# Kernel optimization log

Measured on AMD Instinct MI355X. Metric: run time of the kernel, lower is better.

## Reference

```python
import jax, jax.numpy as jnp
import numpy as np


def setup_inputs() -> dict:
    key = jax.random.key(0)
    k0, k1, k2, k3, k4 = jax.random.split(key, 5)
    B, H, Lq, Lk, D = 2, 8, 512, 512, 32
    q = jax.random.normal(k0, (B, H, Lq, D), dtype=jnp.float32)
    k = jax.random.normal(k1, (B, H, Lk, D), dtype=jnp.float32)
    scale = jnp.ones((1,), dtype=jnp.float32)  # accepted but unused by the module
    # mask True = padded / excluded (torch masked_fill semantics)
    mask = jax.random.bernoulli(k2, 0.1, (B, Lq, Lk))
    attn_bias = jax.random.normal(k3, (B, H, Lq, Lk), dtype=jnp.float32) * 0.1
    # GATv2 attention vector, torch shape (1,H,1,1,D) -> stored as (H,D)
    limit = float(np.sqrt(6.0 / (1.0 + D)))  # xavier_uniform fan_in=1*1*D? torch uses full shape; scale is immaterial for correctness
    attention = jax.random.uniform(k4, (H, D), dtype=jnp.float32, minval=-limit, maxval=limit)
    return {"q": q, "k": k, "scale": scale, "mask": mask, "attn_bias": attn_bias, "attention": attention}


def reference(q, k, scale, mask, attn_bias, attention):
    # q: [B,H,Lq,D], k: [B,H,Lk,D], attention: [H,D]
    # broadcast additive combine -> [B,H,Lq,Lk,D]
    summed = q[:, :, :, None, :] + k[:, :, None, :, :]
    # SiLU activation, dot with per-head attention vector, reduce D -> [B,H,Lq,Lk]
    scores = jnp.einsum("bhqkd,hd->bhqk", jax.nn.silu(summed), attention)
    scores = scores + attn_bias
    # masked softmax over Lk; mask broadcasts over heads (unsqueeze at -3)
    scores = jnp.where(mask[:, None, :, :], -jnp.inf, scores)
    w = jax.nn.softmax(scores, axis=-1)
    # rows that are fully masked produce NaN -> replace with 0 (torch nan_to_num)
    return jnp.nan_to_num(w, nan=0.0)
```

## Files before the change

### kernel.cpp

```cpp
#include <hip/hip_runtime.h>
#include <hip/hip_bf16.h>
#include <math.h>

#define BB 2
#define HH 8
#define LQ 512
#define LK 512
#define DD 32
#define D2 (DD / 2)
#define C2 2
#define NC (D2 / C2)
#define WAVES 8
#define RPW 2
#define ROWSPB (WAVES * RPW)

#define LOG2E 1.44269504088896f

static __device__ __forceinline__ float fast_rcp(float x) {
#if __has_builtin(__builtin_amdgcn_rcpf)
  return __builtin_amdgcn_rcpf(x);
#else
  return 1.0f / x;
#endif
}

static __device__ __forceinline__ float fast_exp2(float x) {
#if __has_builtin(__builtin_amdgcn_exp2f)
  return __builtin_amdgcn_exp2f(x);
#else
  return __expf(x * 0.69314718056f);
#endif
}

__global__ __launch_bounds__(256) void gatv2_prek_p(
    const float* __restrict__ k, const float* __restrict__ att,
    float4* __restrict__ wst4) {
  const int bh = blockIdx.x >> 3;
  const int kt = blockIdx.x & 7;
  const int h = bh & (HH - 1);
  const int t = threadIdx.x;

  __shared__ float tile[64][33];

  const float4* src = (const float4*)(k + ((size_t)bh * LK + kt * 64) * DD);
#pragma unroll
  for (int i = 0; i < 2; ++i) {
    const int idx = t + i * 256;
    const float4 v = src[idx];
    const int kkl = idx >> 3;
    const int d4 = (idx & 7) * 4;
    tile[kkl][d4 + 0] = v.x; tile[kkl][d4 + 1] = v.y;
    tile[kkl][d4 + 2] = v.z; tile[kkl][d4 + 3] = v.w;
  }
  __syncthreads();

  const int d2 = t >> 4;
  const int kl0 = (t & 15) * 4;
  const float a0 = att[h * DD + 2 * d2 + 0];
  const float a1 = att[h * DD + 2 * d2 + 1];
  float4* dst = wst4 + ((size_t)bh * D2 + d2) * LK + kt * 64 + kl0;
#pragma unroll
  for (int j = 0; j < 4; ++j) {
    const float k0 = tile[kl0 + j][2 * d2 + 0];
    const float k1 = tile[kl0 + j][2 * d2 + 1];
    float4 o;
    o.x = fast_exp2(-k0 * LOG2E); o.y = k0 * a0;
    o.z = fast_exp2(-k1 * LOG2E); o.w = k1 * a1;
    dst[j] = o;
  }
}

__global__ __launch_bounds__(512) void gatv2_main_r2(
    const float* __restrict__ q, const int* __restrict__ mask,
    const float* __restrict__ bias, const float* __restrict__ att,
    const float4* __restrict__ wst4, float* __restrict__ out) {
  const int lane = threadIdx.x & 63;
  const int wid = threadIdx.x >> 6;
  const int tid = threadIdx.x;
  const int rowbase = blockIdx.x * ROWSPB;
  const int bh = rowbase >> 9;
  const int b = rowbase >> 12;
  const int h = bh & (HH - 1);

  __shared__ float4 lds4[2][C2 * LK];
  __shared__ float4 cst4[ROWSPB][D2];

  const float4* __restrict__ kb = wst4 + (size_t)bh * (D2 * LK);

  float4 s0 = kb[tid];
  float4 s1 = kb[tid + 512];

  {
    const int rw = wid * RPW + (lane >> 5);
    const int d = lane & 31;
    const float qd = q[(size_t)(rowbase + rw) * DD + d];
    const float ad = att[h * DD + d];
    float2 c;
    c.x = fast_exp2(-qd * LOG2E);
    c.y = qd * ad;
    ((float2*)cst4)[rw * DD + d] = c;
  }
  lds4[0][tid] = s0;
  lds4[0][tid + 512] = s1;

  float acc[RPW][8];
#pragma unroll
  for (int j = 0; j < RPW; ++j)
#pragma unroll
    for (int c = 0; c < 8; ++c) acc[j][c] = 0.0f;

  float bv[RPW][8];
  int mv[RPW][8];

#pragma unroll
  for (int cc = 0; cc < NC; ++cc) {
    __syncthreads();

    float4 s0n, s1n;
    if (cc + 1 < NC) {
      const float4* src = kb + (size_t)(cc + 1) * (C2 * LK);
      s0n = src[tid];
      s1n = src[tid + 512];
    } else {
      const float* __restrict__ brow = bias + (size_t)rowbase * LK;
      const int* __restrict__ mrow = mask + ((size_t)(b * LQ) + (rowbase & (LQ - 1))) * LK;
#pragma unroll
      for (int j = 0; j < RPW; ++j) {
        const int rw = wid * RPW + j;
#pragma unroll
        for (int c = 0; c < 8; ++c) {
          bv[j][c] = brow[(size_t)rw * LK + lane + 64 * c];
          mv[j][c] = mrow[(size_t)rw * LK + lane + 64 * c];
        }
      }
    }

    const float4 c0A = cst4[wid * RPW + 0][cc * 2 + 0];
    const float4 c0B = cst4[wid * RPW + 0][cc * 2 + 1];
    const float4 c1A = cst4[wid * RPW + 1][cc * 2 + 0];
    const float4 c1B = cst4[wid * RPW + 1][cc * 2 + 1];

    const float4* __restrict__ buf = lds4[cc & 1];
#pragma unroll
    for (int d2l = 0; d2l < C2; ++d2l) {
      const float4 k0 = d2l ? c0B : c0A;
      const float4 k1 = d2l ? c1B : c1A;
      const float4* __restrict__ pd = buf + d2l * LK + lane;
#pragma unroll
      for (int c = 0; c < 8; ++c) {
        const float4 p = pd[64 * c];
        float u = fmaf(k0.x, p.x, 1.0f);
        float t = k0.y + p.y;
        acc[0][c] = fmaf(t, fast_rcp(u), acc[0][c]);
        u = fmaf(k0.z, p.z, 1.0f);
        t = k0.w + p.w;
        acc[0][c] = fmaf(t, fast_rcp(u), acc[0][c]);
        u = fmaf(k1.x, p.x, 1.0f);
        t = k1.y + p.y;
        acc[1][c] = fmaf(t, fast_rcp(u), acc[1][c]);
        u = fmaf(k1.z, p.z, 1.0f);
        t = k1.w + p.w;
        acc[1][c] = fmaf(t, fast_rcp(u), acc[1][c]);
      }
    }

    if (cc + 1 < NC) {
      float4* dst = lds4[(cc + 1) & 1];
      dst[tid] = s0n;
      dst[tid + 512] = s1n;
    }
  }

#pragma unroll
  for (int j = 0; j < RPW; ++j) {
    const int r = rowbase + wid * RPW + j;

    float sc[8];
#pragma unroll
    for (int c = 0; c < 8; ++c)
      sc[c] = mv[j][c] ? -INFINITY : (acc[j][c] + bv[j][c]);

    float m = sc[0];
#pragma unroll
    for (int c = 1; c < 8; ++c) m = fmaxf(m, sc[c]);
#pragma unroll
    for (int off = 32; off > 0; off >>= 1)
      m = fmaxf(m, __shfl_xor(m, off, 64));

    float sum = 0.0f;
#pragma unroll
    for (int c = 0; c < 8; ++c) {
      const float p = fast_exp2((sc[c] - m) * LOG2E);
      sc[c] = p;
      sum += p;
    }
#pragma unroll
    for (int off = 32; off > 0; off >>= 1)
      sum += __shfl_xor(sum, off, 64);

    const bool dead = (m == -INFINITY);
    const float inv = dead ? 0.0f : fast_rcp(sum);

    float* __restrict__ orow = out + (size_t)r * LK;
#pragma unroll
    for (int c = 0; c < 8; ++c) {
      orow[lane + 64 * c] = dead ? 0.0f : sc[c] * inv;
    }
  }
}

__global__ __launch_bounds__(256) void gatv2_fallback(
    const float* __restrict__ q, const float* __restrict__ k,
    const int* __restrict__ mask, const float* __restrict__ bias,
    const float* __restrict__ att, float* __restrict__ out) {
  const int lane = threadIdx.x & 63;
  const int wid = threadIdx.x >> 6;
  const int r = blockIdx.x * 4 + wid;
  const int b = r >> 12;
  const int h = (r >> 9) & (HH - 1);
  const int qi = r & (LQ - 1);

  const float* __restrict__ qrow = q + (size_t)r * DD;
  const float* __restrict__ kbase = k + ((size_t)(b * HH + h)) * (size_t)(LK * DD);
  const float* __restrict__ arow = att + h * DD;
  const float* __restrict__ brow = bias + (size_t)r * LK;
  const int* __restrict__ mrow = mask + ((size_t)(b * LQ + qi)) * LK;

  float qv[DD], av[DD];
#pragma unroll
  for (int d0 = 0; d0 < DD; d0 += 4) {
    const float4 qq = *(const float4*)(qrow + d0);
    const float4 aa = *(const float4*)(arow + d0);
    qv[d0 + 0] = qq.x; qv[d0 + 1] = qq.y; qv[d0 + 2] = qq.z; qv[d0 + 3] = qq.w;
    av[d0 + 0] = aa.x; av[d0 + 1] = aa.y; av[d0 + 2] = aa.z; av[d0 + 3] = aa.w;
  }

  float sc[8];
#pragma unroll
  for (int c = 0; c < 8; ++c) {
    const int kk = lane + 64 * c;
    const float* __restrict__ kr = kbase + (size_t)kk * DD;
    const float bval = brow[kk];
    const int mval = mrow[kk];
    float acc = 0.0f;
#pragma unroll
    for (int d0 = 0; d0 < DD; d0 += 4) {
      const float4 kv = *(const float4*)(kr + d0);
      const float kvf[4] = {kv.x, kv.y, kv.z, kv.w};
#pragma unroll
      for (int j = 0; j < 4; ++j) {
        const float t = qv[d0 + j] + kvf[j];
        const float e = fast_exp2(t * -LOG2E);
        const float sg = fast_rcp(1.0f + e);
        acc = fmaf(t * sg, av[d0 + j], acc);
      }
    }
    const float s = acc + bval;
    sc[c] = mval ? -INFINITY : s;
  }

  float m = sc[0];
#pragma unroll
  for (int c = 1; c < 8; ++c) m = fmaxf(m, sc[c]);
#pragma unroll
  for (int off = 32; off > 0; off >>= 1)
    m = fmaxf(m, __shfl_xor(m, off, 64));

  float sum = 0.0f;
#pragma unroll
  for (int c = 0; c < 8; ++c) {
    const float p = fast_exp2((sc[c] - m) * LOG2E);
    sc[c] = p;
    sum += p;
  }
#pragma unroll
  for (int off = 32; off > 0; off >>= 1)
    sum += __shfl_xor(sum, off, 64);

  const bool dead = (m == -INFINITY);
  const float inv = dead ? 0.0f : fast_rcp(sum);

  float* __restrict__ orow = out + (size_t)r * LK;
#pragma unroll
  for (int c = 0; c < 8; ++c) {
    orow[lane + 64 * c] = dead ? 0.0f : sc[c] * inv;
  }
}

extern "C" void kernel_launch(void* const* d_in, const int* in_sizes, int n_in,
                              void* d_out, int out_size, void* d_ws, size_t ws_size,
                              hipStream_t stream) {
  const float* q = (const float*)d_in[0];
  const float* k = (const float*)d_in[1];
  const int* mask = (const int*)d_in[3];
  const float* bias = (const float*)d_in[4];
  const float* att = (const float*)d_in[5];
  float* out = (float*)d_out;

  const int rows = BB * HH * LQ;
  const size_t ws_needed = (size_t)BB * HH * D2 * LK * sizeof(float4);

  if (ws_size >= ws_needed) {
    float4* wst4 = (float4*)d_ws;
    gatv2_prek_p<<<dim3(128), dim3(256), 0, stream>>>(k, att, wst4);
    gatv2_main_r2<<<dim3(rows / ROWSPB), dim3(64 * WAVES), 0, stream>>>(
        q, mask, bias, att, wst4, out);
  } else {
    gatv2_fallback<<<dim3(rows / 4), dim3(256), 0, stream>>>(q, k, mask, bias, att, out);
  }
}
```

Before: 101.1 us.

## Batch four reciprocals into one and process four rows per wave

```diff
diff --git a/kernel.cpp b/kernel.cpp
--- a/kernel.cpp
+++ b/kernel.cpp
@@ -10,8 +10,8 @@
 #define D2 (DD / 2)
 #define C2 2
 #define NC (D2 / C2)
-#define WAVES 8
-#define RPW 2
+#define WAVES 4
+#define RPW 4
 #define ROWSPB (WAVES * RPW)
 
 #define LOG2E 1.44269504088896f
@@ -70,7 +70,7 @@
   }
 }
 
-__global__ __launch_bounds__(512) void gatv2_main_r2(
+__global__ __launch_bounds__(256) void gatv2_main_r4(
     const float* __restrict__ q, const int* __restrict__ mask,
     const float* __restrict__ bias, const float* __restrict__ att,
     const float4* __restrict__ wst4, float* __restrict__ out) {
@@ -83,102 +83,110 @@
   const int h = bh & (HH - 1);
 
   __shared__ float4 lds4[2][C2 * LK];
-  __shared__ float4 cst4[ROWSPB][D2];
+  __shared__ float2 cst2[ROWSPB][DD];
 
   const float4* __restrict__ kb = wst4 + (size_t)bh * (D2 * LK);
 
   float4 s0 = kb[tid];
-  float4 s1 = kb[tid + 512];
-
-  {
-    const int rw = wid * RPW + (lane >> 5);
-    const int d = lane & 31;
+  float4 s1 = kb[tid + 256];
+  float4 s2 = kb[tid + 512];
+  float4 s3 = kb[tid + 768];
+
+#pragma unroll
+  for (int i = 0; i < 2; ++i) {
+    const int idx = tid + i * 256;
+    const int rw = idx >> 5;
+    const int d = idx & 31;
     const float qd = q[(size_t)(rowbase + rw) * DD + d];
     const float ad = att[h * DD + d];
     float2 c;
     c.x = fast_exp2(-qd * LOG2E);
     c.y = qd * ad;
-    ((float2*)cst4)[rw * DD + d] = c;
+    cst2[rw][d] = c;
   }
   lds4[0][tid] = s0;
-  lds4[0][tid + 512] = s1;
+  lds4[0][tid + 256] = s1;
+  lds4[0][tid + 512] = s2;
+  lds4[0][tid + 768] = s3;
 
   float acc[RPW][8];
 #pragma unroll
   for (int j = 0; j < RPW; ++j)
 #pragma unroll
     for (int c = 0; c < 8; ++c) acc[j][c] = 0.0f;
-
-  float bv[RPW][8];
-  int mv[RPW][8];
 
 #pragma unroll
   for (int cc = 0; cc < NC; ++cc) {
     __syncthreads();
 
-    float4 s0n, s1n;
     if (cc + 1 < NC) {
       const float4* src = kb + (size_t)(cc + 1) * (C2 * LK);
-      s0n = src[tid];
-      s1n = src[tid + 512];
-    } else {
-      const float* __restrict__ brow = bias + (size_t)rowbase * LK;
-      const int* __restrict__ mrow = mask + ((size_t)(b * LQ) + (rowbase & (LQ - 1))) * LK;
+      s0 = src[tid];
+      s1 = src[tid + 256];
+      s2 = src[tid + 512];
+      s3 = src[tid + 768];
+    }
+
+    float4 cA[RPW], cB[RPW];
+#pragma unroll
+    for (int j = 0; j < RPW; ++j) {
+      const float2* crow = cst2[wid * RPW + j];
+      cA[j] = *(const float4*)(crow + 4 * cc);
+      cB[j] = *(const float4*)(crow + 4 * cc + 2);
+    }
+
+    const float4* __restrict__ buf = lds4[cc & 1];
+#pragma unroll
+    for (int c = 0; c < 8; ++c) {
+      const float4 p0 = buf[lane + 64 * c];
+      const float4 p1 = buf[LK + lane + 64 * c];
 #pragma unroll
       for (int j = 0; j < RPW; ++j) {
-        const int rw = wid * RPW + j;
-#pragma unroll
-        for (int c = 0; c < 8; ++c) {
-          bv[j][c] = brow[(size_t)rw * LK + lane + 64 * c];
-          mv[j][c] = mrow[(size_t)rw * LK + lane + 64 * c];
-        }
-      }
-    }
-
-    const float4 c0A = cst4[wid * RPW + 0][cc * 2 + 0];
-    const float4 c0B = cst4[wid * RPW + 0][cc * 2 + 1];
-    const float4 c1A = cst4[wid * RPW + 1][cc * 2 + 0];
-    const float4 c1B = cst4[wid * RPW + 1][cc * 2 + 1];
-
-    const float4* __restrict__ buf = lds4[cc & 1];
-#pragma unroll
-    for (int d2l = 0; d2l < C2; ++d2l) {
-      const float4 k0 = d2l ? c0B : c0A;
-      const float4 k1 = d2l ? c1B : c1A;
-      const float4* __restrict__ pd = buf + d2l * LK + lane;
-#pragma unroll
-      for (int c = 0; c < 8; ++c) {
-        const float4 p = pd[64 * c];
-        float u = fmaf(k0.x, p.x, 1.0f);
-        float t = k0.y + p.y;
-        acc[0][c] = fmaf(t, fast_rcp(u), acc[0][c]);
-        u = fmaf(k0.z, p.z, 1.0f);
-        t = k0.w + p.w;
-        acc[0][c] = fmaf(t, fast_rcp(u), acc[0][c]);
-        u = fmaf(k1.x, p.x, 1.0f);
-        t = k1.y + p.y;
-        acc[1][c] = fmaf(t, fast_rcp(u), acc[1][c]);
-        u = fmaf(k1.z, p.z, 1.0f);
-        t = k1.w + p.w;
-        acc[1][c] = fmaf(t, fast_rcp(u), acc[1][c]);
+        const float u0 = fmaf(cA[j].x, p0.x, 1.0f);
+        const float u1 = fmaf(cA[j].z, p0.z, 1.0f);
+        const float u2 = fmaf(cB[j].x, p1.x, 1.0f);
+        const float u3 = fmaf(cB[j].z, p1.z, 1.0f);
+        const float t0 = cA[j].y + p0.y;
+        const float t1 = cA[j].w + p0.w;
+        const float t2 = cB[j].y + p1.y;
+        const float t3 = cB[j].w + p1.w;
+        const float m01 = u0 * u1;
+        const float m23 = u2 * u3;
+        const float r = fast_rcp(m01 * m23);
+        const float r01 = r * m23;
+        const float r23 = r * m01;
+        float a = acc[j][c];
+        a = fmaf(t0, r01 * u1, a);
+        a = fmaf(t1, r01 * u0, a);
+        a = fmaf(t2, r23 * u3, a);
+        a = fmaf(t3, r23 * u2, a);
+        acc[j][c] = a;
       }
     }
 
     if (cc + 1 < NC) {
       float4* dst = lds4[(cc + 1) & 1];
-      dst[tid] = s0n;
-      dst[tid + 512] = s1n;
+      dst[tid] = s0;
+      dst[tid + 256] = s1;
+      dst[tid + 512] = s2;
+      dst[tid + 768] = s3;
     }
   }
 
 #pragma unroll
   for (int j = 0; j < RPW; ++j) {
     const int r = rowbase + wid * RPW + j;
+    const int qi = r & (LQ - 1);
+    const float* __restrict__ brow = bias + (size_t)r * LK;
+    const int* __restrict__ mrow = mask + ((size_t)(b * LQ + qi)) * LK;
 
     float sc[8];
 #pragma unroll
-    for (int c = 0; c < 8; ++c)
-      sc[c] = mv[j][c] ? -INFINITY : (acc[j][c] + bv[j][c]);
+    for (int c = 0; c < 8; ++c) {
+      const float bval = brow[lane + 64 * c];
+      const int mval = mrow[lane + 64 * c];
+      sc[c] = mval ? -INFINITY : (acc[j][c] + bval);
+    }
 
     float m = sc[0];
 #pragma unroll
@@ -303,7 +311,7 @@
   if (ws_size >= ws_needed) {
     float4* wst4 = (float4*)d_ws;
     gatv2_prek_p<<<dim3(128), dim3(256), 0, stream>>>(k, att, wst4);
-    gatv2_main_r2<<<dim3(rows / ROWSPB), dim3(64 * WAVES), 0, stream>>>(
+    gatv2_main_r4<<<dim3(rows / ROWSPB), dim3(64 * WAVES), 0, stream>>>(
         q, mask, bias, att, wst4, out);
   } else {
     gatv2_fallback<<<dim3(rows / 4), dim3(256), 0, stream>>>(q, k, mask, bias, att, out);
```

After: 252.9 us. 2.5x slower.

## Split GATv2 into q/k precompute, register-tiled score kernel, and separate softmax

Applied to the files above, without the earlier changes.

```diff
diff --git a/kernel.cpp b/kernel.cpp
--- a/kernel.cpp
+++ b/kernel.cpp
@@ -7,30 +7,161 @@
 #define LQ 512
 #define LK 512
 #define DD 32
+
+#define LOG2E 1.44269504088896f
+
+static __device__ __forceinline__ float fast_rcp(float x) {
+#if __has_builtin(__builtin_amdgcn_rcpf)
+  return __builtin_amdgcn_rcpf(x);
+#else
+  return 1.0f / x;
+#endif
+}
+
+static __device__ __forceinline__ float fast_exp2(float x) {
+#if __has_builtin(__builtin_amdgcn_exp2f)
+  return __builtin_amdgcn_exp2f(x);
+#else
+  return __expf(x * 0.69314718056f);
+#endif
+}
+
+
+__global__ __launch_bounds__(256) void gatv2_prek_t(
+    const float* __restrict__ k, const float* __restrict__ att,
+    float2* __restrict__ ktab) {
+  const int bh = blockIdx.x >> 3;
+  const int kt = blockIdx.x & 7;
+  const int h = bh & (HH - 1);
+  const int t = threadIdx.x;
+
+  __shared__ float tile[64][33];
+
+  const float4* src = (const float4*)(k + ((size_t)bh * LK + kt * 64) * DD);
+#pragma unroll
+  for (int i = 0; i < 2; ++i) {
+    const int idx = t + i * 256;
+    const float4 v = src[idx];
+    const int kkl = idx >> 3;
+    const int d4 = (idx & 7) * 4;
+    tile[kkl][d4 + 0] = v.x; tile[kkl][d4 + 1] = v.y;
+    tile[kkl][d4 + 2] = v.z; tile[kkl][d4 + 3] = v.w;
+  }
+  __syncthreads();
+
+  const int d = t >> 3;
+  const int kl0 = (t & 7) * 8;
+  const float a = att[h * DD + d];
+  float2* dst = ktab + ((size_t)bh * DD + d) * LK + kt * 64 + kl0;
+#pragma unroll
+  for (int j = 0; j < 8; ++j) {
+    const float kv = tile[kl0 + j][d];
+    float2 o;
+    o.x = fast_exp2(-kv * LOG2E);
+    o.y = kv * a;
+    dst[j] = o;
+  }
+}
+
+__global__ __launch_bounds__(256) void gatv2_prek_q(
+    const float* __restrict__ q, const float* __restrict__ att,
+    float2* __restrict__ qtab) {
+  const int idx = blockIdx.x * 256 + threadIdx.x;
+  const int row = idx >> 5;
+  const int d = idx & 31;
+  const int h = (row >> 9) & (HH - 1);
+  const float qd = q[idx];
+  const float ad = att[h * DD + d];
+  float2 c;
+  c.x = fast_exp2(-qd * LOG2E);
+  c.y = qd * ad;
+  qtab[idx] = c;
+}
+
+__global__ __launch_bounds__(256) void gatv2_score(
+    const float2* __restrict__ ktab, const float2* __restrict__ qtab,
+    const float* __restrict__ bias, const int* __restrict__ mask,
+    float* __restrict__ scores) {
+  const int lane = threadIdx.x & 63;
+  const int w = threadIdx.x >> 6;
+  const int bid = blockIdx.x;
+  const int bh = bid >> 6;
+  const int rem = bid & 63;
+  const int rg = rem >> 1;
+  const int ch = rem & 1;
+  const int col = ch * 256 + w * 64 + lane;
+  const int row0 = bh * LQ + rg * 16;
+  const int b = bh >> 3;
+
+  const float2* __restrict__ kcol = ktab + (size_t)bh * (DD * LK) + col;
+  float2 kf[DD];
+#pragma unroll
+  for (int d = 0; d < DD; ++d) kf[d] = kcol[(size_t)d * LK];
+
+#pragma unroll 2
+  for (int rr = 0; rr < 16; ++rr) {
+    const int row = row0 + rr;
+    const float2* __restrict__ qrow = qtab + (size_t)row * DD;
+    float acc = 0.0f;
+#pragma unroll
+    for (int d = 0; d < DD; ++d) {
+      const float2 qc = qrow[d];
+      const float u = fmaf(qc.x, kf[d].x, 1.0f);
+      const float t = qc.y + kf[d].y;
+      acc = fmaf(t, fast_rcp(u), acc);
+    }
+    const int qi = row & (LQ - 1);
+    const float bval = bias[(size_t)row * LK + col];
+    const int mval = mask[((size_t)(b * LQ + qi)) * LK + col];
+    scores[(size_t)row * LK + col] = mval ? -INFINITY : (acc + bval);
+  }
+}
+
+__global__ __launch_bounds__(256) void gatv2_softmax(
+    const float* __restrict__ scores, float* __restrict__ out) {
+  const int lane = threadIdx.x & 63;
+  const int wid = threadIdx.x >> 6;
+  const int r = blockIdx.x * 4 + wid;
+
+  const float* __restrict__ srow = scores + (size_t)r * LK;
+  float sc[8];
+#pragma unroll
+  for (int c = 0; c < 8; ++c) sc[c] = srow[lane + 64 * c];
+
+  float m = sc[0];
+#pragma unroll
+  for (int c = 1; c < 8; ++c) m = fmaxf(m, sc[c]);
+#pragma unroll
+  for (int off = 32; off > 0; off >>= 1)
+    m = fmaxf(m, __shfl_xor(m, off, 64));
+
+  float sum = 0.0f;
+#pragma unroll
+  for (int c = 0; c < 8; ++c) {
+    const float p = fast_exp2((sc[c] - m) * LOG2E);
+    sc[c] = p;
+    sum += p;
+  }
+#pragma unroll
+  for (int off = 32; off > 0; off >>= 1)
+    sum += __shfl_xor(sum, off, 64);
+
+  const bool dead = (m == -INFINITY);
+  const float inv = dead ? 0.0f : fast_rcp(sum);
+
+  float* __restrict__ orow = out + (size_t)r * LK;
+#pragma unroll
+  for (int c = 0; c < 8; ++c) {
+    orow[lane + 64 * c] = dead ? 0.0f : sc[c] * inv;
+  }
+}
+
 #define D2 (DD / 2)
 #define C2 2
 #define NC (D2 / C2)
 #define WAVES 8
 #define RPW 2
 #define ROWSPB (WAVES * RPW)
-
-#define LOG2E 1.44269504088896f
-
-static __device__ __forceinline__ float fast_rcp(float x) {
-#if __has_builtin(__builtin_amdgcn_rcpf)
-  return __builtin_amdgcn_rcpf(x);
-#else
-  return 1.0f / x;
-#endif
-}
-
-static __device__ __forceinline__ float fast_exp2(float x) {
-#if __has_builtin(__builtin_amdgcn_exp2f)
-  return __builtin_amdgcn_exp2f(x);
-#else
-  return __expf(x * 0.69314718056f);
-#endif
-}
 
 __global__ __launch_bounds__(256) void gatv2_prek_p(
     const float* __restrict__ k, const float* __restrict__ att,
@@ -298,9 +429,21 @@
   float* out = (float*)d_out;
 
   const int rows = BB * HH * LQ;
-  const size_t ws_needed = (size_t)BB * HH * D2 * LK * sizeof(float4);
-
-  if (ws_size >= ws_needed) {
+  const size_t ktab_b = (size_t)BB * HH * DD * LK * sizeof(float2);
+  const size_t qtab_b = (size_t)rows * DD * sizeof(float2);
+  const size_t scores_b = (size_t)rows * LK * sizeof(float);
+
+  if (ws_size >= ktab_b + qtab_b + scores_b) {
+    char* wsb = (char*)d_ws;
+    float2* ktab = (float2*)wsb;
+    float2* qtab = (float2*)(wsb + ktab_b);
+    float* scores = (float*)(wsb + ktab_b + qtab_b);
+
+    gatv2_prek_t<<<dim3(128), dim3(256), 0, stream>>>(k, att, ktab);
+    gatv2_prek_q<<<dim3(1024), dim3(256), 0, stream>>>(q, att, qtab);
+    gatv2_score<<<dim3(1024), dim3(256), 0, stream>>>(ktab, qtab, bias, mask, scores);
+    gatv2_softmax<<<dim3(rows / 4), dim3(256), 0, stream>>>(scores, out);
+  } else if (ws_size >= (size_t)BB * HH * D2 * LK * sizeof(float4)) {
     float4* wst4 = (float4*)d_ws;
     gatv2_prek_p<<<dim3(128), dim3(256), 0, stream>>>(k, att, wst4);
     gatv2_main_r2<<<dim3(rows / ROWSPB), dim3(64 * WAVES), 0, stream>>>(
```

New measurement: 116.6 us. +15.4%, slower.
